# Kernel tuning notes

Measured on AMD Instinct MI355X. Metric: run time of the kernel, lower is better.

Reference implementation:

```python
import jax, jax.numpy as jnp
import numpy as np
from jax.ops import segment_sum

N_NODES = 100000


def gcn_conv(x, edge_index, W, b, n_nodes):
    # PyG GCNConv: add self-loops, symmetric normalization, linear, scatter-add, bias
    src = jnp.concatenate([edge_index[0], jnp.arange(n_nodes, dtype=edge_index.dtype)])
    dst = jnp.concatenate([edge_index[1], jnp.arange(n_nodes, dtype=edge_index.dtype)])
    deg = segment_sum(jnp.ones(src.shape[0], dtype=x.dtype), dst, num_segments=n_nodes)
    dinv = jnp.where(deg > 0, jax.lax.rsqrt(deg), 0.0)
    norm = dinv[src] * dinv[dst]            # [E+N]
    h = x @ W                               # [N, out] dense GEMM first (PyG order)
    msg = h[src] * norm[:, None]            # gather + scale, [E+N, out]
    out = segment_sum(msg, dst, num_segments=n_nodes)  # scatter-add
    return out + b


def setup_inputs() -> dict:
    key = jax.random.key(0)
    k1, k2, k3, k4, k5, k6 = jax.random.split(key, 6)
    in_c, hid_c, out_c = 128, 128, 64
    n_edges = 1600000
    x = jax.random.normal(k1, (N_NODES, in_c), dtype=jnp.float32)
    edge_index = jax.random.randint(k2, (2, n_edges), 0, N_NODES, dtype=jnp.int64)
    # Glorot-ish init for weights, zeros for bias (PyG defaults)
    W1 = jax.random.normal(k3, (in_c, hid_c), dtype=jnp.float32) / np.sqrt(in_c)
    b1 = jnp.zeros((hid_c,), dtype=jnp.float32)
    W2 = jax.random.normal(k4, (hid_c, out_c), dtype=jnp.float32) / np.sqrt(hid_c)
    b2 = jnp.zeros((out_c,), dtype=jnp.float32)
    return {"x": x, "edge_index": edge_index, "W1": W1, "b1": b1, "W2": W2, "b2": b2}


def reference(x, edge_index, W1, b1, W2, b2):
    h = gcn_conv(x, edge_index, W1, b1, N_NODES)
    h = jax.nn.relu(h)
    out = gcn_conv(h, edge_index, W2, b2, N_NODES)
    return out
```

## Files before the change

kernel.cpp:

```cpp
#include <hip/hip_runtime.h>
#include <hip/hip_fp16.h>

#define NN 100000
#define NBKT 196
#define BCAP 16384

using f16x8 = __attribute__((ext_vector_type(8))) _Float16;
using f32x4 = __attribute__((ext_vector_type(4))) float;
using u32x4 = __attribute__((ext_vector_type(4))) unsigned;

__device__ __forceinline__ void fma4(float4& a, float s, const float4& w) {
  a.x = fmaf(s, w.x, a.x);
  a.y = fmaf(s, w.y, a.y);
  a.z = fmaf(s, w.z, a.z);
  a.w = fmaf(s, w.w, a.w);
}

__device__ __forceinline__ void acc8(float* a, float w, uint4 q) {
  const __half2* p = (const __half2*)&q;
#pragma unroll
  for (int j = 0; j < 4; ++j) {
    float2 f = __half22float2(p[j]);
    a[2 * j]     = fmaf(w, f.x, a[2 * j]);
    a[2 * j + 1] = fmaf(w, f.y, a[2 * j + 1]);
  }
}

__device__ __forceinline__ void add8(float* a, uint4 q) {
  const __half2* p = (const __half2*)&q;
#pragma unroll
  for (int j = 0; j < 4; ++j) {
    float2 f = __half22float2(p[j]);
    a[2 * j]     += f.x;
    a[2 * j + 1] += f.y;
  }
}

__device__ __forceinline__ unsigned packh2(float x, float y) {
  __half2 h = __floats2half2_rn(x, y);
  return *(unsigned*)&h;
}

template <int N, bool AHALF, bool PRESCALE>
__device__ __forceinline__ void gemm_body(int bid, const void* __restrict__ Av,
                                          const float* __restrict__ W,
                                          const float* __restrict__ dinv,
                                          _Float16* __restrict__ out, int M,
                                          _Float16* As, _Float16* Bs) {
  constexpr int NF = N / 16;
  const int tid = threadIdx.x;
  const long long row0 = (long long)bid * 64;
  if (AHALF) {
    const _Float16* A = (const _Float16*)Av;
#pragma unroll
    for (int t = 0; t < 4; ++t) {
      int i = tid + t * 256;
      int m = i >> 4, q = i & 15;
      long long row = row0 + m;
      uint4 v = make_uint4(0, 0, 0, 0);
      if (row < M) v = ((const uint4*)A)[row * 16 + q];
      *(uint4*)&As[m * 136 + q * 8] = v;
    }
  } else {
    const float* A = (const float*)Av;
#pragma unroll
    for (int t = 0; t < 8; ++t) {
      int i = tid + t * 256;
      int m = i >> 5, q = i & 31;
      long long row = row0 + m;
      float4 v = make_float4(0.f, 0.f, 0.f, 0.f);
      if (row < M) v = ((const float4*)A)[row * 32 + q];
      uint2 w2 = make_uint2(packh2(v.x, v.y), packh2(v.z, v.w));
      *(uint2*)&As[m * 136 + q * 4] = w2;
    }
  }
#pragma unroll
  for (int t = 0; t < N / 2; ++t) {
    int idx = tid + t * 256;
    int k = idx / N, n = idx % N;
    Bs[n * 136 + k] = (_Float16)W[idx];
  }
  __syncthreads();
  const int lane = tid & 63;
  const int wrow = (tid >> 6) * 16;
  const int r = lane & 15, g = lane >> 4;
  f32x4 acc[NF] = {};
#pragma unroll
  for (int ks = 0; ks < 4; ++ks) {
    f16x8 av = *(const f16x8*)&As[(wrow + r) * 136 + ks * 32 + g * 8];
#pragma unroll
    for (int cf = 0; cf < NF; ++cf) {
      f16x8 bv = *(const f16x8*)&Bs[(cf * 16 + r) * 136 + ks * 32 + g * 8];
      acc[cf] = __builtin_amdgcn_mfma_f32_16x16x32_f16(av, bv, acc[cf], 0, 0, 0);
    }
  }
#pragma unroll
  for (int q = 0; q < 4; ++q) {
    long long row = row0 + wrow + g * 4 + q;
    if (row < M) {
      float sc = PRESCALE ? dinv[row] : 1.0f;
#pragma unroll
      for (int cf = 0; cf < NF; ++cf)
        out[row * N + cf * 16 + r] = (_Float16)(sc * acc[cf][q]);
    }
  }
}

__global__ __launch_bounds__(256) void k_binA_gemm(const int* __restrict__ e,
                                                   int* __restrict__ gcur,
                                                   unsigned int* __restrict__ tmp,
                                                   int E, int nA,
                                                   const float* __restrict__ x,
                                                   const float* __restrict__ W1,
                                                   _Float16* __restrict__ hh,
                                                   int M) {
  __shared__ char smem[52224];
  const int b = blockIdx.x;
  const int tid = threadIdx.x;
  if (b >= nA) {
    _Float16* As = (_Float16*)smem;
    _Float16* Bs = (_Float16*)(smem + 64 * 136 * 2);
    gemm_body<128, false, false>(b - nA, x, W1, nullptr, hh, M, As, Bs);
    return;
  }
  int* cnt = (int*)smem;
  int* pcur = cnt + 256;
  int* sm_flag = pcur + 256;
  cnt[tid] = 0;
  if (tid < 64) {
    int n64 = E < 64 ? E : 64;
    int odd = (tid < n64) ? e[2 * tid + 1] : 0;
    unsigned long long nz = __ballot(odd != 0);
    if (tid == 0) *sm_flag = (nz == 0ull) ? 1 : 0;
  }
  __syncthreads();
  const int m = *sm_flag;
  const bool pok = ((E & 1) == 0);
  const int start = b * 4096;
  int ss[16], dd[16];
#pragma unroll
  for (int k = 0; k < 8; ++k) {
    int i = start + 2 * (tid + k * 256);
    int s0 = -1, s1 = -1, d0 = 0, d1 = 0;
    if (i < E) {
      if (m) {
        if (pok) {
          int4 sp = ((const int4*)e)[i >> 1];
          int4 dp = ((const int4*)e)[(E + i) >> 1];
          s0 = sp.x; s1 = sp.z; d0 = dp.x; d1 = dp.z;
        } else {
          s0 = (int)((const long long*)e)[i];
          d0 = (int)((const long long*)e)[E + i];
          if (i + 1 < E) {
            s1 = (int)((const long long*)e)[i + 1];
            d1 = (int)((const long long*)e)[E + i + 1];
          }
        }
      } else {
        if (pok) {
          int2 sp = ((const int2*)e)[i >> 1];
          int2 dp = ((const int2*)(e + E))[i >> 1];
          s0 = sp.x; s1 = sp.y; d0 = dp.x; d1 = dp.y;
        } else {
          s0 = e[i]; d0 = e[E + i];
          if (i + 1 < E) { s1 = e[i + 1]; d1 = e[E + i + 1]; }
        }
      }
      if (i + 1 >= E) s1 = -1;
      atomicAdd(&cnt[d0 >> 9], 1);
      if (s1 >= 0) atomicAdd(&cnt[d1 >> 9], 1);
    }
    ss[2 * k] = s0; dd[2 * k] = d0;
    ss[2 * k + 1] = s1; dd[2 * k + 1] = d1;
  }
  __syncthreads();
  if (tid < NBKT && cnt[tid] > 0)
    pcur[tid] = tid * BCAP + atomicAdd(&gcur[tid], cnt[tid]);
  __syncthreads();
#pragma unroll
  for (int k = 0; k < 16; ++k) {
    if (ss[k] >= 0) {
      int bk = dd[k] >> 9;
      int p = atomicAdd(&pcur[bk], 1);
      tmp[p] = ((unsigned)ss[k] << 9) | (unsigned)(dd[k] & 511);
    }
  }
}

__global__ __launch_bounds__(256) void k_gemm2(const _Float16* __restrict__ A,
                                               const float* __restrict__ W2,
                                               const float* __restrict__ dinv,
                                               _Float16* __restrict__ out, int M) {
  __shared__ _Float16 As[64 * 136];
  __shared__ _Float16 Bs[64 * 136];
  gemm_body<64, true, true>(blockIdx.x, A, W2, dinv, out, M, As, Bs);
}

__global__ __launch_bounds__(256) void k_binB(const unsigned int* __restrict__ tmp,
                                              const int* __restrict__ gcur,
                                              int* __restrict__ rowptr,
                                              float* __restrict__ dinv,
                                              int* __restrict__ srcs) {
  __shared__ int sbuf[256];
  __shared__ int hist[512];
  __shared__ int lofs[512];
  const int b = blockIdx.x;
  const int tid = threadIdx.x;
  int c = (tid < NBKT) ? gcur[tid] : 0;
  sbuf[tid] = c;
  __syncthreads();
#pragma unroll
  for (int off = 1; off < 256; off <<= 1) {
    int t = (tid >= off) ? sbuf[tid - off] : 0;
    __syncthreads();
    sbuf[tid] += t;
    __syncthreads();
  }
  const int total = sbuf[255];
  const int incl = sbuf[b];
  const int base_b = (b > 0) ? sbuf[b - 1] : 0;
  const int cntb = incl - base_b;
  if (b == 0 && tid == 0) rowptr[NN] = total;
  __syncthreads();
  hist[tid] = 0;
  hist[tid + 256] = 0;
  __syncthreads();
  const int tbeg = b * BCAP;
  const int tend = tbeg + cntb;
  for (int j = tbeg + tid; j < tend; j += 256) atomicAdd(&hist[tmp[j] & 511], 1);
  __syncthreads();
  int a0 = hist[2 * tid], a1 = hist[2 * tid + 1];
  int sv = a0 + a1;
  sbuf[tid] = sv;
  __syncthreads();
#pragma unroll
  for (int off = 1; off < 256; off <<= 1) {
    int t = (tid >= off) ? sbuf[tid - off] : 0;
    __syncthreads();
    sbuf[tid] += t;
    __syncthreads();
  }
  int excl = sbuf[tid] - sv;
  lofs[2 * tid] = excl;
  lofs[2 * tid + 1] = excl + a0;
  __syncthreads();
  for (int i = tid; i < 512; i += 256) {
    int node = (b << 9) + i;
    if (node < NN) {
      rowptr[node] = base_b + lofs[i];
      dinv[node] = rsqrtf((float)(hist[i] + 1));
    }
  }
  __syncthreads();
  for (int j = tbeg + tid; j < tend; j += 256) {
    unsigned v = tmp[j];
    int p = base_b + atomicAdd(&lofs[v & 511], 1);
    srcs[p] = (int)(v >> 9);
  }
}

__global__ __launch_bounds__(256) void k_gather1(const int* __restrict__ rowptr,
                                                 const int* __restrict__ srcs,
                                                 const float* __restrict__ dinv,
                                                 const _Float16* __restrict__ h,
                                                 const float* __restrict__ b,
                                                 _Float16* __restrict__ out) {
  constexpr int C = 128;
  const int wave = threadIdx.x >> 6;
  const int lane = threadIdx.x & 63;
  const int grp = lane >> 4;
  const int li = lane & 15;
  const int node = blockIdx.x * 16 + wave * 4 + grp;
  if (node >= NN) return;
  const float dd = dinv[node];
  float acc[8];
  {
    uint4 q = *(const uint4*)(h + (long long)node * C + li * 8);
    const __half2* p = (const __half2*)&q;
#pragma unroll
    for (int j = 0; j < 4; ++j) {
      float2 f = __half22float2(p[j]);
      acc[2 * j]     = dd * f.x;
      acc[2 * j + 1] = dd * f.y;
    }
  }
  const int beg = rowptr[node], end = rowptr[node + 1];
  int e = beg;
  for (; e + 4 <= end; e += 4) {
    int s0 = __builtin_nontemporal_load(srcs + e);
    int s1 = __builtin_nontemporal_load(srcs + e + 1);
    int s2 = __builtin_nontemporal_load(srcs + e + 2);
    int s3 = __builtin_nontemporal_load(srcs + e + 3);
    float w0 = dinv[s0], w1 = dinv[s1], w2 = dinv[s2], w3 = dinv[s3];
    uint4 q0 = *(const uint4*)(h + (long long)s0 * C + li * 8);
    uint4 q1 = *(const uint4*)(h + (long long)s1 * C + li * 8);
    uint4 q2 = *(const uint4*)(h + (long long)s2 * C + li * 8);
    uint4 q3 = *(const uint4*)(h + (long long)s3 * C + li * 8);
    acc8(acc, w0, q0);
    acc8(acc, w1, q1);
    acc8(acc, w2, q2);
    acc8(acc, w3, q3);
  }
  for (; e < end; ++e) {
    int s0 = __builtin_nontemporal_load(srcs + e);
    float w0 = dinv[s0];
    uint4 q0 = *(const uint4*)(h + (long long)s0 * C + li * 8);
    acc8(acc, w0, q0);
  }
  const float4* b4 = (const float4*)b;
  float4 bb0 = b4[li * 2], bb1 = b4[li * 2 + 1];
  float o[8];
  o[0] = fmaf(dd, acc[0], bb0.x);
  o[1] = fmaf(dd, acc[1], bb0.y);
  o[2] = fmaf(dd, acc[2], bb0.z);
  o[3] = fmaf(dd, acc[3], bb0.w);
  o[4] = fmaf(dd, acc[4], bb1.x);
  o[5] = fmaf(dd, acc[5], bb1.y);
  o[6] = fmaf(dd, acc[6], bb1.z);
  o[7] = fmaf(dd, acc[7], bb1.w);
#pragma unroll
  for (int j = 0; j < 8; ++j) o[j] = fmaxf(o[j], 0.f);
  u32x4 w;
  w.x = packh2(o[0], o[1]);
  w.y = packh2(o[2], o[3]);
  w.z = packh2(o[4], o[5]);
  w.w = packh2(o[6], o[7]);
  __builtin_nontemporal_store(w, (u32x4*)(out + (long long)node * C + li * 8));
}

__global__ __launch_bounds__(256) void k_gather2(const int* __restrict__ rowptr,
                                                 const int* __restrict__ srcs,
                                                 const float* __restrict__ dinv,
                                                 const _Float16* __restrict__ h,
                                                 const float* __restrict__ b,
                                                 float* __restrict__ out) {
  constexpr int C = 64;
  const int wave = threadIdx.x >> 6;
  const int lane = threadIdx.x & 63;
  const int grp = lane >> 3;
  const int li = lane & 7;
  const int node = blockIdx.x * 32 + wave * 8 + grp;
  if (node >= NN) return;
  const float dd = dinv[node];
  float acc[8];
  {
    uint4 q = *(const uint4*)(h + (long long)node * C + li * 8);
    const __half2* p = (const __half2*)&q;
#pragma unroll
    for (int j = 0; j < 4; ++j) {
      float2 f = __half22float2(p[j]);
      acc[2 * j]     = f.x;
      acc[2 * j + 1] = f.y;
    }
  }
  const int beg = rowptr[node], end = rowptr[node + 1];
  int e = beg;
  for (; e + 4 <= end; e += 4) {
    int s0 = __builtin_nontemporal_load(srcs + e);
    int s1 = __builtin_nontemporal_load(srcs + e + 1);
    int s2 = __builtin_nontemporal_load(srcs + e + 2);
    int s3 = __builtin_nontemporal_load(srcs + e + 3);
    uint4 q0 = *(const uint4*)(h + (long long)s0 * C + li * 8);
    uint4 q1 = *(const uint4*)(h + (long long)s1 * C + li * 8);
    uint4 q2 = *(const uint4*)(h + (long long)s2 * C + li * 8);
    uint4 q3 = *(const uint4*)(h + (long long)s3 * C + li * 8);
    add8(acc, q0);
    add8(acc, q1);
    add8(acc, q2);
    add8(acc, q3);
  }
  for (; e < end; ++e) {
    uint4 q0 = *(const uint4*)(h + (long long)__builtin_nontemporal_load(srcs + e) * C + li * 8);
    add8(acc, q0);
  }
  const float4* b4 = (const float4*)b;
  float4 bb0 = b4[li * 2], bb1 = b4[li * 2 + 1];
  float* op = out + (long long)node * C + li * 8;
  f32x4 v0, v1;
  v0.x = fmaf(dd, acc[0], bb0.x);
  v0.y = fmaf(dd, acc[1], bb0.y);
  v0.z = fmaf(dd, acc[2], bb0.z);
  v0.w = fmaf(dd, acc[3], bb0.w);
  v1.x = fmaf(dd, acc[4], bb1.x);
  v1.y = fmaf(dd, acc[5], bb1.y);
  v1.z = fmaf(dd, acc[6], bb1.z);
  v1.w = fmaf(dd, acc[7], bb1.w);
  __builtin_nontemporal_store(v0, (f32x4*)op);
  __builtin_nontemporal_store(v1, (f32x4*)(op + 4));
}

__global__ void k_zero_i32(int* p, int n) {
  int i = blockIdx.x * 256 + threadIdx.x;
  if (i < n) p[i] = 0;
}

__global__ void k_detect_f(const int* __restrict__ e, int* flag, int E) {
  if (threadIdx.x == 0 && blockIdx.x == 0) {
    int n = E < 64 ? E : 64;
    int m = 1;
    for (int i = 0; i < n; ++i)
      if (e[2 * i + 1] != 0) { m = 0; break; }
    *flag = m;
  }
}

__global__ void k_deg_count(const int* __restrict__ e, const int* __restrict__ flag,
                            int* __restrict__ deg, int E) {
  int i = blockIdx.x * 256 + threadIdx.x;
  if (i >= E) return;
  int m = *flag;
  int d = m ? e[2 * (E + i)] : e[E + i];
  atomicAdd(&deg[d], 1);
}

__global__ void k_dinv_f(const int* __restrict__ deg, float* __restrict__ dinv) {
  int i = blockIdx.x * 256 + threadIdx.x;
  if (i < NN) dinv[i] = rsqrtf((float)(deg[i] + 1));
}

template <int N, bool RELU>
__global__ __launch_bounds__(256) void k_gemm_v(const float* __restrict__ A,
                                                const float* __restrict__ W,
                                                float* __restrict__ out, int M) {
  constexpr int K4 = 32;
  constexpr int N4 = N / 4;
  constexpr int CG = N4;
  constexpr int ROWS = (256 / CG) * 4;
  __shared__ float4 Wl[128 * N4];
  __shared__ float4 Xl[ROWS * K4];
  const int tid = threadIdx.x;
  const float4* W4 = (const float4*)W;
  for (int i = tid; i < 128 * N4; i += 256) Wl[i] = W4[i];
  const long long row0 = (long long)blockIdx.x * ROWS;
  const float4* A4 = (const float4*)A;
  for (int i = tid; i < ROWS * K4; i += 256) {
    int r = i >> 5;
    long long row = row0 + r;
    float4 v = make_float4(0.f, 0.f, 0.f, 0.f);
    if (row < M) v = A4[row * K4 + (i & 31)];
    if (RELU) {
      v.x = fmaxf(v.x, 0.f); v.y = fmaxf(v.y, 0.f);
      v.z = fmaxf(v.z, 0.f); v.w = fmaxf(v.w, 0.f);
    }
    Xl[i] = v;
  }
  __syncthreads();
  const int c = tid % CG;
  const int rb = (tid / CG) * 4;
  float4 a0 = make_float4(0, 0, 0, 0), a1 = a0, a2 = a0, a3 = a0;
#pragma unroll 4
  for (int k4 = 0; k4 < K4; ++k4) {
    float4 w0 = Wl[(k4 * 4 + 0) * N4 + c];
    float4 w1 = Wl[(k4 * 4 + 1) * N4 + c];
    float4 w2 = Wl[(k4 * 4 + 2) * N4 + c];
    float4 w3 = Wl[(k4 * 4 + 3) * N4 + c];
    float4 x0 = Xl[(rb + 0) * K4 + k4];
    float4 x1 = Xl[(rb + 1) * K4 + k4];
    float4 x2 = Xl[(rb + 2) * K4 + k4];
    float4 x3 = Xl[(rb + 3) * K4 + k4];
    fma4(a0, x0.x, w0); fma4(a0, x0.y, w1); fma4(a0, x0.z, w2); fma4(a0, x0.w, w3);
    fma4(a1, x1.x, w0); fma4(a1, x1.y, w1); fma4(a1, x1.z, w2); fma4(a1, x1.w, w3);
    fma4(a2, x2.x, w0); fma4(a2, x2.y, w1); fma4(a2, x2.z, w2); fma4(a2, x2.w, w3);
    fma4(a3, x3.x, w0); fma4(a3, x3.y, w1); fma4(a3, x3.z, w2); fma4(a3, x3.w, w3);
  }
  float4* O4 = (float4*)out;
  long long row = row0 + rb;
  if (row + 0 < M) O4[(row + 0) * N4 + c] = a0;
  if (row + 1 < M) O4[(row + 1) * N4 + c] = a1;
  if (row + 2 < M) O4[(row + 2) * N4 + c] = a2;
  if (row + 3 < M) O4[(row + 3) * N4 + c] = a3;
}

template <int C>
__global__ void k_self_bias(const float* __restrict__ h, const float* __restrict__ dinv,
                            const float* __restrict__ b, float* __restrict__ out) {
  constexpr int C4 = C / 4;
  int gid = blockIdx.x * 256 + threadIdx.x;
  if (gid >= NN * C4) return;
  int node = gid / C4;
  int cq = gid % C4;
  float di = dinv[node];
  float sc = di * di;
  float4 v = ((const float4*)h)[gid];
  float4 bb = ((const float4*)b)[cq];
  float4 o;
  o.x = fmaf(v.x, sc, bb.x);
  o.y = fmaf(v.y, sc, bb.y);
  o.z = fmaf(v.z, sc, bb.z);
  o.w = fmaf(v.w, sc, bb.w);
  ((float4*)out)[gid] = o;
}

template <int C>
__global__ void k_scatter(const int* __restrict__ e, const int* __restrict__ flag,
                          const float* __restrict__ dinv, const float* __restrict__ h,
                          float* __restrict__ out, int E) {
  constexpr int TPE = C / 4;
  long long gid = (long long)blockIdx.x * blockDim.x + threadIdx.x;
  int ei = (int)(gid / TPE);
  int cq = (int)(gid % TPE);
  if (ei >= E) return;
  int m = *flag;
  int s, d;
  if (m) { s = e[2 * ei]; d = e[2 * (E + ei)]; }
  else   { s = e[ei];     d = e[E + ei]; }
  float nrm = dinv[s] * dinv[d];
  float4 v = ((const float4*)h)[(long long)s * TPE + cq];
  float* op = out + (long long)d * C + (long long)cq * 4;
  unsafeAtomicAdd(op + 0, v.x * nrm);
  unsafeAtomicAdd(op + 1, v.y * nrm);
  unsafeAtomicAdd(op + 2, v.z * nrm);
  unsafeAtomicAdd(op + 3, v.w * nrm);
}

extern "C" void kernel_launch(void* const* d_in, const int* in_sizes, int n_in,
                              void* d_out, int out_size, void* d_ws, size_t ws_size,
                              hipStream_t stream) {
  const float* x  = (const float*)d_in[0];
  const int*   e  = (const int*)d_in[1];
  const float* W1 = (const float*)d_in[2];
  const float* b1 = (const float*)d_in[3];
  const float* W2 = (const float*)d_in[4];
  const float* b2 = (const float*)d_in[5];
  float* out = (float*)d_out;
  const int E = in_sizes[1] / 2;

  char* ws = (char*)d_ws;
  const size_t o_flag    = 0;
  const size_t o_dinv    = 16;
  const size_t o_rowptr  = 400016;
  const size_t o_gcur    = 800032;
  const size_t o_tmp     = 800832;
  const size_t o_srcs    = 13645888;
  const size_t o_h       = 20045888;
  const size_t o_out1    = 45645888;
  const size_t need_csr  = 71245888;

  int*      flag   = (int*)(ws + o_flag);
  float*    dinv   = (float*)(ws + o_dinv);
  int*      rowptr = (int*)(ws + o_rowptr);
  int*      gcur   = (int*)(ws + o_gcur);
  unsigned* tmp    = (unsigned*)(ws + o_tmp);
  int*      srcs   = (int*)(ws + o_srcs);
  _Float16* hh     = (_Float16*)(ws + o_h);
  _Float16* out1   = (_Float16*)(ws + o_out1);

  if (ws_size >= need_csr) {
    const int nA = (E + 4095) / 4096;
    const int nG = (NN + 63) / 64;
    (void)hipMemsetAsync(gcur, 0, NBKT * sizeof(int), stream);
    k_binA_gemm<<<nA + nG, 256, 0, stream>>>(e, gcur, tmp, E, nA, x, W1, hh, NN);
    k_binB<<<NBKT, 256, 0, stream>>>(tmp, gcur, rowptr, dinv, srcs);
    k_gather1<<<(NN + 15) / 16, 256, 0, stream>>>(rowptr, srcs, dinv, hh, b1, out1);
    k_gemm2<<<nG, 256, 0, stream>>>(out1, W2, dinv, hh, NN);
    k_gather2<<<(NN + 31) / 32, 256, 0, stream>>>(rowptr, srcs, dinv, hh, b2, out);
  } else {
    int*   deg   = (int*)(ws + 400016);
    float* hF    = (float*)(ws + (1 << 20));
    float* out1F = (float*)(ws + (1 << 20) + 51200000);
    k_detect_f<<<1, 64, 0, stream>>>(e, flag, E);
    k_zero_i32<<<(NN + 255) / 256, 256, 0, stream>>>(deg, NN);
    k_deg_count<<<(E + 255) / 256, 256, 0, stream>>>(e, flag, deg, E);
    k_dinv_f<<<(NN + 255) / 256, 256, 0, stream>>>(deg, dinv);
    k_gemm_v<128, false><<<(NN + 31) / 32, 256, 0, stream>>>(x, W1, hF, NN);
    k_self_bias<128><<<(NN * 32 + 255) / 256, 256, 0, stream>>>(hF, dinv, b1, out1F);
    long long tot1 = (long long)E * 32;
    k_scatter<128><<<(int)((tot1 + 255) / 256), 256, 0, stream>>>(e, flag, dinv, hF, out1F, E);
    k_gemm_v<64, true><<<(NN + 63) / 64, 256, 0, stream>>>(out1F, W2, hF, NN);
    k_self_bias<64><<<(NN * 16 + 255) / 256, 256, 0, stream>>>(hF, dinv, b2, out);
    long long tot2 = (long long)E * 16;
    k_scatter<64><<<(int)((tot2 + 255) / 256), 256, 0, stream>>>(e, flag, dinv, hF, out, E);
  }
}
```

Baseline: 228.9 us.

## Prescale layer-1 GEMM output by dinv and fuse GEMM1 with CSR build

Node degrees are now counted with global atomics during edge binning and turned into dinv by a separate small kernel. This lets the first GEMM run alongside the CSR-finalize kernel and scale its output rows by dinv. The layer-1 gather can then sum neighbour rows without loading dinv for each edge. The cost is 1.6M extra global atomics on a degree array plus one more kernel launch, and the GEMM no longer overlaps with the binning pass.

```diff
diff --git a/kernel.cpp b/kernel.cpp
--- a/kernel.cpp
+++ b/kernel.cpp
@@ -14,16 +14,6 @@
   a.y = fmaf(s, w.y, a.y);
   a.z = fmaf(s, w.z, a.z);
   a.w = fmaf(s, w.w, a.w);
-}
-
-__device__ __forceinline__ void acc8(float* a, float w, uint4 q) {
-  const __half2* p = (const __half2*)&q;
-#pragma unroll
-  for (int j = 0; j < 4; ++j) {
-    float2 f = __half22float2(p[j]);
-    a[2 * j]     = fmaf(w, f.x, a[2 * j]);
-    a[2 * j + 1] = fmaf(w, f.y, a[2 * j + 1]);
-  }
 }
 
 __device__ __forceinline__ void add8(float* a, uint4 q) {
@@ -106,35 +96,25 @@
   }
 }
 
-__global__ __launch_bounds__(256) void k_binA_gemm(const int* __restrict__ e,
-                                                   int* __restrict__ gcur,
-                                                   unsigned int* __restrict__ tmp,
-                                                   int E, int nA,
-                                                   const float* __restrict__ x,
-                                                   const float* __restrict__ W1,
-                                                   _Float16* __restrict__ hh,
-                                                   int M) {
-  __shared__ char smem[52224];
+__global__ __launch_bounds__(256) void k_binA(const int* __restrict__ e,
+                                              int* __restrict__ gcur,
+                                              int* __restrict__ deg,
+                                              unsigned int* __restrict__ tmp,
+                                              int E) {
+  __shared__ int cnt[256];
+  __shared__ int pcur[256];
+  __shared__ int sm_flag;
   const int b = blockIdx.x;
   const int tid = threadIdx.x;
-  if (b >= nA) {
-    _Float16* As = (_Float16*)smem;
-    _Float16* Bs = (_Float16*)(smem + 64 * 136 * 2);
-    gemm_body<128, false, false>(b - nA, x, W1, nullptr, hh, M, As, Bs);
-    return;
-  }
-  int* cnt = (int*)smem;
-  int* pcur = cnt + 256;
-  int* sm_flag = pcur + 256;
   cnt[tid] = 0;
   if (tid < 64) {
     int n64 = E < 64 ? E : 64;
     int odd = (tid < n64) ? e[2 * tid + 1] : 0;
     unsigned long long nz = __ballot(odd != 0);
-    if (tid == 0) *sm_flag = (nz == 0ull) ? 1 : 0;
-  }
-  __syncthreads();
-  const int m = *sm_flag;
+    if (tid == 0) sm_flag = (nz == 0ull) ? 1 : 0;
+  }
+  __syncthreads();
+  const int m = sm_flag;
   const bool pok = ((E & 1) == 0);
   const int start = b * 4096;
   int ss[16], dd[16];
@@ -168,7 +148,11 @@
       }
       if (i + 1 >= E) s1 = -1;
       atomicAdd(&cnt[d0 >> 9], 1);
-      if (s1 >= 0) atomicAdd(&cnt[d1 >> 9], 1);
+      atomicAdd(&deg[d0], 1);
+      if (s1 >= 0) {
+        atomicAdd(&cnt[d1 >> 9], 1);
+        atomicAdd(&deg[d1], 1);
+      }
     }
     ss[2 * k] = s0; dd[2 * k] = d0;
     ss[2 * k + 1] = s1; dd[2 * k + 1] = d1;
@@ -184,6 +168,81 @@
       int p = atomicAdd(&pcur[bk], 1);
       tmp[p] = ((unsigned)ss[k] << 9) | (unsigned)(dd[k] & 511);
     }
+  }
+}
+
+__global__ void k_dinv(const int* __restrict__ deg, float* __restrict__ dinv) {
+  int i = blockIdx.x * 256 + threadIdx.x;
+  if (i < NN) dinv[i] = rsqrtf((float)(deg[i] + 1));
+}
+
+__global__ __launch_bounds__(256) void k_binB_gemm1(const unsigned int* __restrict__ tmp,
+                                                    const int* __restrict__ gcur,
+                                                    int* __restrict__ rowptr,
+                                                    int* __restrict__ srcs,
+                                                    const float* __restrict__ x,
+                                                    const float* __restrict__ W1,
+                                                    const float* __restrict__ dinv,
+                                                    _Float16* __restrict__ hh, int M) {
+  __shared__ char smem[52224];
+  const int b = blockIdx.x;
+  const int tid = threadIdx.x;
+  if (b >= NBKT) {
+    _Float16* As = (_Float16*)smem;
+    _Float16* Bs = (_Float16*)(smem + 64 * 136 * 2);
+    gemm_body<128, false, true>(b - NBKT, x, W1, dinv, hh, M, As, Bs);
+    return;
+  }
+  int* sbuf = (int*)smem;
+  int* hist = sbuf + 256;
+  int* lofs = hist + 512;
+  int c = (tid < NBKT) ? gcur[tid] : 0;
+  sbuf[tid] = c;
+  __syncthreads();
+#pragma unroll
+  for (int off = 1; off < 256; off <<= 1) {
+    int t = (tid >= off) ? sbuf[tid - off] : 0;
+    __syncthreads();
+    sbuf[tid] += t;
+    __syncthreads();
+  }
+  const int total = sbuf[255];
+  const int incl = sbuf[b];
+  const int base_b = (b > 0) ? sbuf[b - 1] : 0;
+  const int cntb = incl - base_b;
+  if (b == 0 && tid == 0) rowptr[NN] = total;
+  __syncthreads();
+  hist[tid] = 0;
+  hist[tid + 256] = 0;
+  __syncthreads();
+  const int tbeg = b * BCAP;
+  const int tend = tbeg + cntb;
+  for (int j = tbeg + tid; j < tend; j += 256) atomicAdd(&hist[tmp[j] & 511], 1);
+  __syncthreads();
+  int a0 = hist[2 * tid], a1 = hist[2 * tid + 1];
+  int sv = a0 + a1;
+  sbuf[tid] = sv;
+  __syncthreads();
+#pragma unroll
+  for (int off = 1; off < 256; off <<= 1) {
+    int t = (tid >= off) ? sbuf[tid - off] : 0;
+    __syncthreads();
+    sbuf[tid] += t;
+    __syncthreads();
+  }
+  int excl = sbuf[tid] - sv;
+  lofs[2 * tid] = excl;
+  lofs[2 * tid + 1] = excl + a0;
+  __syncthreads();
+  for (int i = tid; i < 512; i += 256) {
+    int node = (b << 9) + i;
+    if (node < NN) rowptr[node] = base_b + lofs[i];
+  }
+  __syncthreads();
+  for (int j = tbeg + tid; j < tend; j += 256) {
+    unsigned v = tmp[j];
+    int p = base_b + atomicAdd(&lofs[v & 511], 1);
+    srcs[p] = (int)(v >> 9);
   }
 }
 
@@ -194,69 +253,6 @@
   __shared__ _Float16 As[64 * 136];
   __shared__ _Float16 Bs[64 * 136];
   gemm_body<64, true, true>(blockIdx.x, A, W2, dinv, out, M, As, Bs);
-}
-
-__global__ __launch_bounds__(256) void k_binB(const unsigned int* __restrict__ tmp,
-                                              const int* __restrict__ gcur,
-                                              int* __restrict__ rowptr,
-                                              float* __restrict__ dinv,
-                                              int* __restrict__ srcs) {
-  __shared__ int sbuf[256];
-  __shared__ int hist[512];
-  __shared__ int lofs[512];
-  const int b = blockIdx.x;
-  const int tid = threadIdx.x;
-  int c = (tid < NBKT) ? gcur[tid] : 0;
-  sbuf[tid] = c;
-  __syncthreads();
-#pragma unroll
-  for (int off = 1; off < 256; off <<= 1) {
-    int t = (tid >= off) ? sbuf[tid - off] : 0;
-    __syncthreads();
-    sbuf[tid] += t;
-    __syncthreads();
-  }
-  const int total = sbuf[255];
-  const int incl = sbuf[b];
-  const int base_b = (b > 0) ? sbuf[b - 1] : 0;
-  const int cntb = incl - base_b;
-  if (b == 0 && tid == 0) rowptr[NN] = total;
-  __syncthreads();
-  hist[tid] = 0;
-  hist[tid + 256] = 0;
-  __syncthreads();
-  const int tbeg = b * BCAP;
-  const int tend = tbeg + cntb;
-  for (int j = tbeg + tid; j < tend; j += 256) atomicAdd(&hist[tmp[j] & 511], 1);
-  __syncthreads();
-  int a0 = hist[2 * tid], a1 = hist[2 * tid + 1];
-  int sv = a0 + a1;
-  sbuf[tid] = sv;
-  __syncthreads();
-#pragma unroll
-  for (int off = 1; off < 256; off <<= 1) {
-    int t = (tid >= off) ? sbuf[tid - off] : 0;
-    __syncthreads();
-    sbuf[tid] += t;
-    __syncthreads();
-  }
-  int excl = sbuf[tid] - sv;
-  lofs[2 * tid] = excl;
-  lofs[2 * tid + 1] = excl + a0;
-  __syncthreads();
-  for (int i = tid; i < 512; i += 256) {
-    int node = (b << 9) + i;
-    if (node < NN) {
-      rowptr[node] = base_b + lofs[i];
-      dinv[node] = rsqrtf((float)(hist[i] + 1));
-    }
-  }
-  __syncthreads();
-  for (int j = tbeg + tid; j < tend; j += 256) {
-    unsigned v = tmp[j];
-    int p = base_b + atomicAdd(&lofs[v & 511], 1);
-    srcs[p] = (int)(v >> 9);
-  }
 }
 
 __global__ __launch_bounds__(256) void k_gather1(const int* __restrict__ rowptr,
@@ -280,8 +276,8 @@
 #pragma unroll
     for (int j = 0; j < 4; ++j) {
       float2 f = __half22float2(p[j]);
-      acc[2 * j]     = dd * f.x;
-      acc[2 * j + 1] = dd * f.y;
+      acc[2 * j]     = f.x;
+      acc[2 * j + 1] = f.y;
     }
   }
   const int beg = rowptr[node], end = rowptr[node + 1];
@@ -291,21 +287,19 @@
     int s1 = __builtin_nontemporal_load(srcs + e + 1);
     int s2 = __builtin_nontemporal_load(srcs + e + 2);
     int s3 = __builtin_nontemporal_load(srcs + e + 3);
-    float w0 = dinv[s0], w1 = dinv[s1], w2 = dinv[s2], w3 = dinv[s3];
     uint4 q0 = *(const uint4*)(h + (long long)s0 * C + li * 8);
     uint4 q1 = *(const uint4*)(h + (long long)s1 * C + li * 8);
     uint4 q2 = *(const uint4*)(h + (long long)s2 * C + li * 8);
     uint4 q3 = *(const uint4*)(h + (long long)s3 * C + li * 8);
-    acc8(acc, w0, q0);
-    acc8(acc, w1, q1);
-    acc8(acc, w2, q2);
-    acc8(acc, w3, q3);
+    add8(acc, q0);
+    add8(acc, q1);
+    add8(acc, q2);
+    add8(acc, q3);
   }
   for (; e < end; ++e) {
     int s0 = __builtin_nontemporal_load(srcs + e);
-    float w0 = dinv[s0];
     uint4 q0 = *(const uint4*)(h + (long long)s0 * C + li * 8);
-    acc8(acc, w0, q0);
+    add8(acc, q0);
   }
   const float4* b4 = (const float4*)b;
   float4 bb0 = b4[li * 2], bb1 = b4[li * 2 + 1];
@@ -529,16 +523,18 @@
   const size_t o_flag    = 0;
   const size_t o_dinv    = 16;
   const size_t o_rowptr  = 400016;
-  const size_t o_gcur    = 800032;
-  const size_t o_tmp     = 800832;
-  const size_t o_srcs    = 13645888;
-  const size_t o_h       = 20045888;
-  const size_t o_out1    = 45645888;
-  const size_t need_csr  = 71245888;
+  const size_t o_deg     = 800032;
+  const size_t o_gcur    = 1200032;
+  const size_t o_tmp     = 1200832;
+  const size_t o_srcs    = 14045888;
+  const size_t o_h       = 20445888;
+  const size_t o_out1    = 46045888;
+  const size_t need_csr  = 71645888;
 
   int*      flag   = (int*)(ws + o_flag);
   float*    dinv   = (float*)(ws + o_dinv);
   int*      rowptr = (int*)(ws + o_rowptr);
+  int*      deg    = (int*)(ws + o_deg);
   int*      gcur   = (int*)(ws + o_gcur);
   unsigned* tmp    = (unsigned*)(ws + o_tmp);
   int*      srcs   = (int*)(ws + o_srcs);
@@ -548,20 +544,22 @@
   if (ws_size >= need_csr) {
     const int nA = (E + 4095) / 4096;
     const int nG = (NN + 63) / 64;
-    (void)hipMemsetAsync(gcur, 0, NBKT * sizeof(int), stream);
-    k_binA_gemm<<<nA + nG, 256, 0, stream>>>(e, gcur, tmp, E, nA, x, W1, hh, NN);
-    k_binB<<<NBKT, 256, 0, stream>>>(tmp, gcur, rowptr, dinv, srcs);
+    (void)hipMemsetAsync(deg, 0, 400000 + 800, stream);
+    k_binA<<<nA, 256, 0, stream>>>(e, gcur, deg, tmp, E);
+    k_dinv<<<(NN + 255) / 256, 256, 0, stream>>>(deg, dinv);
+    k_binB_gemm1<<<NBKT + nG, 256, 0, stream>>>(tmp, gcur, rowptr, srcs,
+                                                x, W1, dinv, hh, NN);
     k_gather1<<<(NN + 15) / 16, 256, 0, stream>>>(rowptr, srcs, dinv, hh, b1, out1);
     k_gemm2<<<nG, 256, 0, stream>>>(out1, W2, dinv, hh, NN);
     k_gather2<<<(NN + 31) / 32, 256, 0, stream>>>(rowptr, srcs, dinv, hh, b2, out);
   } else {
-    int*   deg   = (int*)(ws + 400016);
+    int*   degF  = (int*)(ws + 400016);
     float* hF    = (float*)(ws + (1 << 20));
     float* out1F = (float*)(ws + (1 << 20) + 51200000);
     k_detect_f<<<1, 64, 0, stream>>>(e, flag, E);
-    k_zero_i32<<<(NN + 255) / 256, 256, 0, stream>>>(deg, NN);
-    k_deg_count<<<(E + 255) / 256, 256, 0, stream>>>(e, flag, deg, E);
-    k_dinv_f<<<(NN + 255) / 256, 256, 0, stream>>>(deg, dinv);
+    k_zero_i32<<<(NN + 255) / 256, 256, 0, stream>>>(degF, NN);
+    k_deg_count<<<(E + 255) / 256, 256, 0, stream>>>(e, flag, degF, E);
+    k_dinv_f<<<(NN + 255) / 256, 256, 0, stream>>>(degF, dinv);
     k_gemm_v<128, false><<<(NN + 31) / 32, 256, 0, stream>>>(x, W1, hF, NN);
     k_self_bias<128><<<(NN * 32 + 255) / 256, 256, 0, stream>>>(hF, dinv, b1, out1F);
     long long tot1 = (long long)E * 32;
```

Measured after the change: 272.5 us. 19.1% more time.
